# Optimization experiments

Measured on AMD Instinct MI355X. Metric: run time of the kernel, lower is better.

The kernel has to match this reference:

```python
import jax, jax.numpy as jnp
import numpy as np

N, E, IN = 50000, 800000, 128   # nodes, edges, input feature dim
H, C = 8, 32                    # heads, per-head channels
HC = H * C                      # 256 = concat width
NEG_SLOPE = 0.2
BN_EPS = 1e-5


def _gat_conv(x, src, dst, W, a_src, a_dst, b, heads, out_ch, concat):
    """PyG-style GATConv (eval mode, self-loops already in src/dst)."""
    n = x.shape[0]
    h = (x @ W).reshape(n, heads, out_ch)                 # [N,H,C]
    alpha_s = (h * a_src).sum(-1)                         # [N,H]
    alpha_d = (h * a_dst).sum(-1)                         # [N,H]
    e = jax.nn.leaky_relu(alpha_s[src] + alpha_d[dst], NEG_SLOPE)  # [Etot,H]
    # segment softmax over destination nodes (every node has a self-loop)
    emax = jax.ops.segment_max(e, dst, num_segments=n)    # [N,H]
    e = jnp.exp(e - emax[dst])
    denom = jax.ops.segment_sum(e, dst, num_segments=n)
    alpha = e / (denom[dst] + 1e-16)                      # [Etot,H]
    msg = h[src] * alpha[:, :, None]                      # [Etot,H,C]
    out = jax.ops.segment_sum(msg, dst, num_segments=n)   # [N,H,C]
    out = out.reshape(n, heads * out_ch) if concat else out.mean(axis=1)
    return out + b


def _bn(y, g, beta, m, v):
    return (y - m) * jax.lax.rsqrt(v + BN_EPS) * g + beta


def setup_inputs() -> dict:
    key = jax.random.key(0)
    ks = jax.random.split(key, 32)
    def p(i, shape, s=0.1):
        return jax.random.normal(ks[i], shape, dtype=jnp.float32) * s
    x = jax.random.normal(ks[0], (N, IN), dtype=jnp.float32)
    edge_index = jax.random.randint(ks[1], (2, E), 0, N, dtype=jnp.int32)
    d = dict(
        x=x, edge_index=edge_index,
        W1=p(2, (IN, HC)), a_src1=p(3, (H, C)), a_dst1=p(4, (H, C)), b1=p(5, (HC,)),
        bn1_g=jnp.ones((HC,), jnp.float32), bn1_b=jnp.zeros((HC,), jnp.float32),
        bn1_m=p(6, (HC,)), bn1_v=jax.random.uniform(ks[7], (HC,), jnp.float32, 0.5, 1.5),
        W2=p(8, (HC, HC)), a_src2=p(9, (H, C)), a_dst2=p(10, (H, C)), b2=p(11, (HC,)),
        bn2_g=jnp.ones((HC,), jnp.float32), bn2_b=jnp.zeros((HC,), jnp.float32),
        bn2_m=p(12, (HC,)), bn2_v=jax.random.uniform(ks[13], (HC,), jnp.float32, 0.5, 1.5),
        W3=p(14, (HC, C)), a_src3=p(15, (1, C)), a_dst3=p(16, (1, C)), b3=p(17, (C,)),
        Ws1=p(18, (IN, HC)), bs1=p(19, (HC,)),
        Ws2=p(20, (HC, C)), bs2=p(21, (C,)),
    )
    return d


def reference(x, edge_index, W1, a_src1, a_dst1, b1, bn1_g, bn1_b, bn1_m, bn1_v,
              W2, a_src2, a_dst2, b2, bn2_g, bn2_b, bn2_m, bn2_v,
              W3, a_src3, a_dst3, b3, Ws1, bs1, Ws2, bs2):
    n = x.shape[0]
    loops = jnp.arange(n, dtype=edge_index.dtype)
    src = jnp.concatenate([edge_index[0], loops])   # PyG add_self_loops=True
    dst = jnp.concatenate([edge_index[1], loops])
    x0 = x @ Ws1 + bs1                               # skip1
    h = _gat_conv(x, src, dst, W1, a_src1, a_dst1, b1, H, C, True)
    h = jax.nn.elu(_bn(h, bn1_g, bn1_b, bn1_m, bn1_v)) + x0
    xs = h @ Ws2 + bs2                               # skip2
    h2 = _gat_conv(h, src, dst, W2, a_src2, a_dst2, b2, H, C, True)
    h2 = jax.nn.elu(_bn(h2, bn2_g, bn2_b, bn2_m, bn2_v))
    out = _gat_conv(h2, src, dst, W3, a_src3, a_dst3, b3, 1, C, False) + xs
    return out
```

## Files before the change

### kernel.cpp

```cpp
#include <hip/hip_runtime.h>
#include <hip/hip_bf16.h>

#define NEG_SLOPE 0.2f
#define BN_EPS 1e-5f
#define BSH 8
#define STASH_CAP 6400

typedef __attribute__((ext_vector_type(8))) short bf16x8;
typedef __attribute__((ext_vector_type(4))) float f32x4;
typedef __attribute__((ext_vector_type(2))) float f32x2;

#if defined(__has_builtin)
#if __has_builtin(__builtin_amdgcn_cvt_f32_fp8) && __has_builtin(__builtin_amdgcn_cvt_pk_fp8_f32)
#define HW_FP8 1
#endif
#if __has_builtin(__builtin_amdgcn_cvt_pk_f32_fp8)
#define HW_FP8_PK 1
#endif
#endif

__device__ __forceinline__ float bf2f(unsigned short u) {
    union { unsigned int i; float f; } x;
    x.i = ((unsigned int)u) << 16;
    return x.f;
}
__device__ __forceinline__ unsigned short f2bf(float f) {
    __hip_bfloat16 b = __float2bfloat16(f);
    return *reinterpret_cast<unsigned short*>(&b);
}
__device__ __forceinline__ float lrelu(float v) {
    return v > 0.f ? v : NEG_SLOPE * v;
}
__device__ __forceinline__ void gload_lds16(const void* g, void* l) {
    __builtin_amdgcn_global_load_lds(
        (const __attribute__((address_space(1))) unsigned int*)(g),
        (__attribute__((address_space(3))) unsigned int*)(l),
        16, 0, 0);
}

__device__ __forceinline__ unsigned char f8enc(float f) {
#ifdef HW_FP8
    int p = __builtin_amdgcn_cvt_pk_fp8_f32(f, 0.f, 0, false);
    return (unsigned char)(p & 0xff);
#else
    float a = fabsf(f);
    unsigned int sign = (__float_as_uint(f) >> 31) << 7;
    if (a < 0.0009765625f) return (unsigned char)sign;
    a = fminf(a, 448.f);
    unsigned int bits = __float_as_uint(a);
    int e = (int)((bits >> 23) & 0xff) - 127;
    unsigned int mant = bits & 0x7fffff;
    if (e < -6) {
        int q = (int)(a * 512.f + 0.5f);
        if (q >= 8) return (unsigned char)(sign | 0x08);
        return (unsigned char)(sign | q);
    }
    unsigned int m = mant >> 20;
    unsigned int rem = mant & 0xfffff;
    if (rem > 0x80000 || (rem == 0x80000 && (m & 1))) m++;
    if (m == 8) { m = 0; e++; }
    if (e > 8) { e = 8; m = 6; }
    return (unsigned char)(sign | ((unsigned int)(e + 7) << 3) | m);
#endif
}
template <int SEL>
__device__ __forceinline__ float f8dec(unsigned int w) {
#ifdef HW_FP8
    return __builtin_amdgcn_cvt_f32_fp8(w, SEL);
#else
    unsigned int b = (w >> (SEL * 8)) & 0xff;
    unsigned int s = b >> 7, em = b & 0x7f;
    float mag;
    if (em >= 8) {
        unsigned int bits = (((em >> 3) + 120) << 23) | ((em & 7) << 20);
        mag = __uint_as_float(bits);
    } else {
        mag = (float)em * 0.001953125f;
    }
    return s ? -mag : mag;
#endif
}
__device__ __forceinline__ void fma_f8x4(float we, unsigned int wv, float4& acc) {
#ifdef HW_FP8_PK
    f32x2 lo = __builtin_amdgcn_cvt_pk_f32_fp8((int)wv, false);
    f32x2 hi = __builtin_amdgcn_cvt_pk_f32_fp8((int)wv, true);
    acc.x = fmaf(we, lo[0], acc.x);
    acc.y = fmaf(we, lo[1], acc.y);
    acc.z = fmaf(we, hi[0], acc.z);
    acc.w = fmaf(we, hi[1], acc.w);
#else
    acc.x = fmaf(we, f8dec<0>(wv), acc.x);
    acc.y = fmaf(we, f8dec<1>(wv), acc.y);
    acc.z = fmaf(we, f8dec<2>(wv), acc.z);
    acc.w = fmaf(we, f8dec<3>(wv), acc.w);
#endif
}

__device__ __forceinline__ int block_scan_incl(int v, int t) {
    int lane = t & 63, w = t >> 6;
    int sv = v;
    #pragma unroll
    for (int off = 1; off < 64; off <<= 1) {
        int u = __shfl_up(sv, off);
        if (lane >= off) sv += u;
    }
    __shared__ int ws_[4];
    if (lane == 63) ws_[w] = sv;
    __syncthreads();
    if (t == 0) {
        int a = 0;
        #pragma unroll
        for (int k = 0; k < 4; k++) { int x = ws_[k]; ws_[k] = a; a += x; }
    }
    __syncthreads();
    return sv + ws_[w];
}

__global__ __launch_bounds__(256) void phase1(const int* __restrict__ dstl,
                                              int E, int N, int NB,
                                              int* __restrict__ gHist,
                                              const float* __restrict__ x,
                                              unsigned short* __restrict__ xb, int n4x,
                                              const float* __restrict__ W1,
                                              const float* __restrict__ Ws1,
                                              const float* __restrict__ W2,
                                              const float* __restrict__ Ws2,
                                              const float* __restrict__ W3,
                                              const float* __restrict__ a_src1,
                                              const float* __restrict__ a_dst1,
                                              const float* __restrict__ a_src2,
                                              const float* __restrict__ a_dst2,
                                              const float* __restrict__ a_src3,
                                              const float* __restrict__ a_dst3,
                                              unsigned short* __restrict__ Wcat1,
                                              unsigned short* __restrict__ Wcat2,
                                              unsigned short* __restrict__ W3t) {
    int t = threadIdx.x;
    if (blockIdx.x < 256) {
        __shared__ int h[256];
        h[t] = 0;
        __syncthreads();
        int Etot = E + N;
        for (int i = blockIdx.x * 256 + t; i < Etot; i += 256 * 256) {
            int d = (i < E) ? dstl[i] : (i - E);
            atomicAdd(&h[d >> BSH], 1);
        }
        __syncthreads();
        if (t < NB && h[t]) atomicAdd(&gHist[t], h[t]);
        return;
    }
    int i = (blockIdx.x - 256) * 256 + t;
    if (i < n4x) {
        float4 v = reinterpret_cast<const float4*>(x)[i];
        ushort4 o;
        o.x = f2bf(v.x); o.y = f2bf(v.y); o.z = f2bf(v.z); o.w = f2bf(v.w);
        reinterpret_cast<ushort4*>(xb)[i] = o;
        return;
    }
    int j = i - n4x;
    if (j < 32768) {
        int m = j >> 7, k = j & 127;
        Wcat1[j] = f2bf(W1[k * 256 + m]);
    } else if (j < 65536) {
        int q = j - 32768; int m = q >> 7, k = q & 127;
        Wcat1[32768 + q] = f2bf(Ws1[k * 256 + m]);
    } else if (j < 131072) {
        int q = j - 65536; int m = q >> 8, k = q & 255;
        Wcat2[q] = f2bf(W2[k * 256 + m]);
    } else if (j < 139264) {
        int q = j - 131072; int m = q >> 8, k = q & 255;
        Wcat2[65536 + q] = f2bf(Ws2[k * 32 + m]);
    } else if (j < 147456) {
        int q = j - 139264; int m = q >> 8, k = q & 255;
        W3t[q] = f2bf(W3[k * 32 + m]);
    } else if (j < 149504) {
        int q = j - 147456; int r = q >> 7, k = q & 127;
        int h = r & 7;
        const float* av = (r < 8) ? a_src1 : a_dst1;
        float s = 0.f;
        #pragma unroll
        for (int c = 0; c < 32; c++) s += W1[k * 256 + h * 32 + c] * av[h * 32 + c];
        Wcat1[(512 + r) * 128 + k] = f2bf(s);
    } else if (j < 153600) {
        int q = j - 149504; int r = q >> 8, k = q & 255;
        int h = r & 7;
        const float* av = (r < 8) ? a_src2 : a_dst2;
        float s = 0.f;
        #pragma unroll
        for (int c = 0; c < 32; c++) s += W2[k * 256 + h * 32 + c] * av[h * 32 + c];
        Wcat2[(288 + r) * 256 + k] = f2bf(s);
    } else if (j < 154112) {
        int q = j - 153600; int r = q >> 8, k = q & 255;
        const float* av = r ? a_dst3 : a_src3;
        float s = 0.f;
        #pragma unroll
        for (int c = 0; c < 32; c++) s += W3[k * 32 + c] * av[c];
        W3t[(32 + r) * 256 + k] = f2bf(s);
    }
}

__global__ __launch_bounds__(256) void bucket_scatter(const int* __restrict__ srcl,
                                                      const int* __restrict__ dstl,
                                                      int E, int N, int NB,
                                                      const int* __restrict__ gHist,
                                                      int* __restrict__ gCursor,
                                                      unsigned int* __restrict__ bktEdges) {
    __shared__ unsigned int stage[4096];
    __shared__ int lbase[256];
    __shared__ int hist[256];
    __shared__ int bexcl[257];
    __shared__ int curk[256];
    __shared__ int gbase[256];
    int t = threadIdx.x;
    int Etot = E + N;
    int begin = blockIdx.x * 4096;

    int gv = (t < NB) ? gHist[t] : 0;
    int gincl = block_scan_incl(gv, t);
    lbase[t] = gincl - gv;
    __syncthreads();

    hist[t] = 0;
    __syncthreads();

    unsigned int ent[16];
    int eb[16];
    #pragma unroll
    for (int k = 0; k < 16; k++) {
        int i = begin + k * 256 + t;
        if (i < Etot) {
            int s, d;
            if (i < E) { s = srcl[i]; d = dstl[i]; }
            else       { s = d = i - E; }
            eb[k] = d >> BSH;
            ent[k] = ((unsigned int)s << BSH) | (unsigned int)(d & 255);
            atomicAdd(&hist[eb[k]], 1);
        } else eb[k] = -1;
    }
    __syncthreads();

    int v = hist[t];
    int incl = block_scan_incl(v, t);
    bexcl[t] = incl - v;
    curk[t] = incl - v;
    if (t == 255) bexcl[256] = incl;
    __syncthreads();

    #pragma unroll
    for (int k = 0; k < 16; k++) {
        if (eb[k] >= 0) {
            int slot = atomicAdd(&curk[eb[k]], 1);
            stage[slot] = ent[k];
        }
    }
    if (t < NB) {
        int cnt = hist[t];
        gbase[t] = cnt ? (lbase[t] + atomicAdd(&gCursor[t], cnt)) : 0;
    }
    __syncthreads();

    int total = bexcl[256];
    for (int p = t; p < total; p += 256) {
        int lo = 0, hi = NB - 1;
        while (lo < hi) {
            int mid = (lo + hi + 1) >> 1;
            if (bexcl[mid] <= p) lo = mid; else hi = mid - 1;
        }
        bktEdges[gbase[lo] + (p - bexcl[lo])] = stage[p];
    }
}

__global__ __launch_bounds__(256) void bucket_to_csr(const unsigned int* __restrict__ bktEdges,
                                                     const int* __restrict__ gHist,
                                                     int* __restrict__ indptr,
                                                     int* __restrict__ esrc,
                                                     int N, int NB, int Etot) {
    __shared__ int lbase[256];
    __shared__ int nh[256];
    __shared__ int ncur[256];
    __shared__ unsigned int stash[STASH_CAP];
    int b = blockIdx.x, t = threadIdx.x;

    int gv = (t < NB) ? gHist[t] : 0;
    int gincl = block_scan_incl(gv, t);
    lbase[t] = gincl - gv;
    __syncthreads();
    int base = lbase[b];
    int cnt = gHist[b];
    int nodeBase = b << BSH;

    nh[t] = 0;
    __syncthreads();
    for (int p = t; p < cnt; p += 256) {
        unsigned int e = bktEdges[base + p];
        if (p < STASH_CAP) stash[p] = e;
        atomicAdd(&nh[e & 255], 1);
    }
    __syncthreads();
    int v = nh[t];
    int incl = block_scan_incl(v, t);
    int excl = incl - v;
    ncur[t] = excl;
    if (nodeBase + t < N) indptr[nodeBase + t] = base + excl;
    __syncthreads();
    for (int p = t; p < cnt; p += 256) {
        unsigned int e = (p < STASH_CAP) ? stash[p] : bktEdges[base + p];
        int slot = atomicAdd(&ncur[e & 255], 1);
        esrc[base + slot] = (int)(e >> BSH);
    }
    if (b == 0 && t == 0) indptr[N] = Etot;
}

template <int K, int COLS>
__global__ __launch_bounds__(256) void gemm_panel(const unsigned short* __restrict__ A,
                                                  const unsigned short* __restrict__ Bt,
                                                  unsigned short* __restrict__ outBf,
                                                  unsigned char* __restrict__ outQ,
                                                  unsigned short* __restrict__ outSk,
                                                  const float* __restrict__ biasSk,
                                                  float* __restrict__ asOut,
                                                  float* __restrict__ adOut,
                                                  int M, int NCtot,
                                                  int split, int split2,
                                                  int ldBf, int ldSk) {
    constexpr int KS = K / 32;
    constexpr int NJ = COLS / 16;
    constexpr int BYTES = COLS * K * 2;
    constexpr int RB = (K == 128) ? 8 : 9;
    __shared__ __align__(16) char lds[BYTES];

    int t = threadIdx.x;
    int w = t >> 6, lane = t & 63;
    int l16 = lane & 15, quad = lane >> 4;
    int rowBase = blockIdx.x * 64 + w * 16;
    int colBase = blockIdx.y * COLS;

    bf16x8 af[KS];
    {
        int gr = rowBase + l16; if (gr >= M) gr = M - 1;
        const unsigned short* aP = A + (size_t)gr * K + quad * 8;
        #pragma unroll
        for (int ks = 0; ks < KS; ks++)
            af[ks] = *reinterpret_cast<const bf16x8*>(aP + ks * 32);
    }

    {
        const char* bSrc = reinterpret_cast<const char*>(Bt + (size_t)colBase * K);
        #pragma unroll
        for (int i = 0; i < BYTES / 4096; i++) {
            int a = (i * 256 + t) * 16;
            int g = a ^ (((a >> RB) & 15) << 4);
            gload_lds16(bSrc + g, &lds[a]);
        }
    }
    __syncthreads();

    f32x4 acc[NJ];
    #pragma unroll
    for (int j = 0; j < NJ; j++) acc[j] = (f32x4){0.f, 0.f, 0.f, 0.f};

    #pragma unroll
    for (int j = 0; j < NJ; j++) {
        int base = (j * 16 + l16) * (K * 2) + quad * 16;
        #pragma unroll
        for (int ks = 0; ks < KS; ks++) {
            int addr = (base + ks * 64) ^ (l16 << 4);
            bf16x8 b = *reinterpret_cast<const bf16x8*>(&lds[addr]);
            acc[j] = __builtin_amdgcn_mfma_f32_16x16x32_bf16(af[ks], b, acc[j], 0, 0, 0);
        }
    }

    #pragma unroll
    for (int j = 0; j < NJ; j++) {
        int c = colBase + j * 16 + l16;
        if (c >= NCtot) continue;
        if (c < split) {
            #pragma unroll
            for (int r = 0; r < 4; r++) {
                int row = rowBase + quad * 4 + r;
                if (row >= M) continue;
                float v = acc[j][r];
                if (outBf) outBf[(size_t)row * ldBf + c] = f2bf(v);
                if (outQ)  outQ[(size_t)row * ldBf + c] = f8enc(v);
            }
        } else if (c < split2) {
            float bv = biasSk[c - split];
            #pragma unroll
            for (int r = 0; r < 4; r++) {
                int row = rowBase + quad * 4 + r;
                if (row >= M) continue;
                outSk[(size_t)row * ldSk + (c - split)] = f2bf(acc[j][r] + bv);
            }
        } else {
            int a = c - split2;
            #pragma unroll
            for (int r = 0; r < 4; r++) {
                int row = rowBase + quad * 4 + r;
                if (row >= M) continue;
                float v = acc[j][r];
                if (NCtot - split2 == 16) {
                    if (a < 8) asOut[(size_t)row * 8 + a] = v;
                    else       adOut[(size_t)row * 8 + a - 8] = v;
                } else {
                    if (a == 0) asOut[row] = v;
                    else        adOut[row] = v;
                }
            }
        }
    }
}

template <int MODE>
__global__ __launch_bounds__(256) void agg256(const unsigned char* __restrict__ hq,
                                              const float* __restrict__ as,
                                              const float* __restrict__ ad,
                                              const int* __restrict__ indptr,
                                              const int* __restrict__ esrc,
                                              const float* __restrict__ bias,
                                              const float* __restrict__ bn_g,
                                              const float* __restrict__ bn_b,
                                              const float* __restrict__ bn_m,
                                              const float* __restrict__ bn_v,
                                              const unsigned short* __restrict__ skip,
                                              unsigned short* __restrict__ out, int N) {
    int t = threadIdx.x;
    int n = blockIdx.x * 4 + (t >> 6);
    if (n >= N) return;
    int lane = t & 63;
    int e8 = lane >> 3, h8 = lane & 7;
    int g4 = lane >> 4, cl = lane & 15;
    int hd = cl >> 1;
    int start = indptr[n], end = indptr[n + 1];
    int cnt = end - start;

    float adh = ad[n * 8 + h8];
    const unsigned char* hqc = hq + cl * 16;

    float4 acc0 = make_float4(0.f, 0.f, 0.f, 0.f);
    float4 acc1 = make_float4(0.f, 0.f, 0.f, 0.f);
    float4 acc2 = make_float4(0.f, 0.f, 0.f, 0.f);
    float4 acc3 = make_float4(0.f, 0.f, 0.f, 0.f);
    float sm = 0.f;
    int nfull = cnt & ~7;

    int sA = 0, sB = 0;
    float wA = 0.f, wB = 0.f;
    uint4 hv0 = {}, hv1 = {};
    if (nfull) {
        sA = esrc[start + e8];
        wA = __expf(lrelu(as[sA * 8 + h8] + adh));
        int r0 = __shfl(sA, g4 * 8);
        int r1 = __shfl(sA, (4 + g4) * 8);
        hv0 = *reinterpret_cast<const uint4*>(hqc + (size_t)r0 * 256);
        hv1 = *reinterpret_cast<const uint4*>(hqc + (size_t)r1 * 256);
        if (nfull > 8) {
            sB = esrc[start + 8 + e8];
            wB = __expf(lrelu(as[sB * 8 + h8] + adh));
        }
    }
    for (int i0 = start; i0 < start + nfull; i0 += 8) {
        uint4 u0 = hv0, u1 = hv1;
        float wcur = wA;
        if (i0 + 8 < start + nfull) {
            int r0 = __shfl(sB, g4 * 8);
            int r1 = __shfl(sB, (4 + g4) * 8);
            hv0 = *reinterpret_cast<const uint4*>(hqc + (size_t)r0 * 256);
            hv1 = *reinterpret_cast<const uint4*>(hqc + (size_t)r1 * 256);
        }
        sA = sB; wA = wB;
        if (i0 + 16 < start + nfull) {
            sB = esrc[i0 + 16 + e8];
            wB = __expf(lrelu(as[sB * 8 + h8] + adh));
        }
        sm += wcur;
        float w0 = __shfl(wcur, g4 * 8 + hd);
        float w1 = __shfl(wcur, (4 + g4) * 8 + hd);
        fma_f8x4(w0, u0.x, acc0);
        fma_f8x4(w0, u0.y, acc1);
        fma_f8x4(w0, u0.z, acc2);
        fma_f8x4(w0, u0.w, acc3);
        fma_f8x4(w1, u1.x, acc0);
        fma_f8x4(w1, u1.y, acc1);
        fma_f8x4(w1, u1.z, acc2);
        fma_f8x4(w1, u1.w, acc3);
    }
    int rem = cnt - nfull;
    if (rem) {
        int i0 = start + nfull;
        int idx = i0 + e8;
        bool valid = idx < end;
        int s_r = esrc[valid ? idx : end - 1];
        float w_r = valid ? __expf(lrelu(as[s_r * 8 + h8] + adh)) : 0.f;
        sm += w_r;
        int r0 = __shfl(s_r, g4 * 8);
        uint4 u0 = *reinterpret_cast<const uint4*>(hqc + (size_t)r0 * 256);
        float w0 = __shfl(w_r, g4 * 8 + hd);
        fma_f8x4(w0, u0.x, acc0);
        fma_f8x4(w0, u0.y, acc1);
        fma_f8x4(w0, u0.z, acc2);
        fma_f8x4(w0, u0.w, acc3);
        if (rem > 4) {
            int r1 = __shfl(s_r, (4 + g4) * 8);
            uint4 u1 = *reinterpret_cast<const uint4*>(hqc + (size_t)r1 * 256);
            float w1 = __shfl(w_r, (4 + g4) * 8 + hd);
            fma_f8x4(w1, u1.x, acc0);
            fma_f8x4(w1, u1.y, acc1);
            fma_f8x4(w1, u1.z, acc2);
            fma_f8x4(w1, u1.w, acc3);
        }
    }

    acc0.x += __shfl_xor(acc0.x, 16); acc0.y += __shfl_xor(acc0.y, 16);
    acc0.z += __shfl_xor(acc0.z, 16); acc0.w += __shfl_xor(acc0.w, 16);
    acc0.x += __shfl_xor(acc0.x, 32); acc0.y += __shfl_xor(acc0.y, 32);
    acc0.z += __shfl_xor(acc0.z, 32); acc0.w += __shfl_xor(acc0.w, 32);
    acc1.x += __shfl_xor(acc1.x, 16); acc1.y += __shfl_xor(acc1.y, 16);
    acc1.z += __shfl_xor(acc1.z, 16); acc1.w += __shfl_xor(acc1.w, 16);
    acc1.x += __shfl_xor(acc1.x, 32); acc1.y += __shfl_xor(acc1.y, 32);
    acc1.z += __shfl_xor(acc1.z, 32); acc1.w += __shfl_xor(acc1.w, 32);
    acc2.x += __shfl_xor(acc2.x, 16); acc2.y += __shfl_xor(acc2.y, 16);
    acc2.z += __shfl_xor(acc2.z, 16); acc2.w += __shfl_xor(acc2.w, 16);
    acc2.x += __shfl_xor(acc2.x, 32); acc2.y += __shfl_xor(acc2.y, 32);
    acc2.z += __shfl_xor(acc2.z, 32); acc2.w += __shfl_xor(acc2.w, 32);
    acc3.x += __shfl_xor(acc3.x, 16); acc3.y += __shfl_xor(acc3.y, 16);
    acc3.z += __shfl_xor(acc3.z, 16); acc3.w += __shfl_xor(acc3.w, 16);
    acc3.x += __shfl_xor(acc3.x, 32); acc3.y += __shfl_xor(acc3.y, 32);
    acc3.z += __shfl_xor(acc3.z, 32); acc3.w += __shfl_xor(acc3.w, 32);

    #pragma unroll
    for (int off = 8; off < 64; off <<= 1) sm += __shfl_xor(sm, off);
    float il = 1.f / (sm + 1e-16f);
    float il_c = __shfl(il, hd);

    float4 my;
    if (g4 == 0)      my = acc0;
    else if (g4 == 1) my = acc1;
    else if (g4 == 2) my = acc2;
    else              my = acc3;
    int cb = cl * 16 + g4 * 4;

    float4 bv  = *reinterpret_cast<const float4*>(&bias[cb]);
    float4 gv  = *reinterpret_cast<const float4*>(&bn_g[cb]);
    float4 bbv = *reinterpret_cast<const float4*>(&bn_b[cb]);
    float4 mv  = *reinterpret_cast<const float4*>(&bn_m[cb]);
    float4 vv  = *reinterpret_cast<const float4*>(&bn_v[cb]);
    float o[4] = {my.x * il_c + bv.x, my.y * il_c + bv.y,
                  my.z * il_c + bv.z, my.w * il_c + bv.w};
    float g[4] = {gv.x, gv.y, gv.z, gv.w}, bb[4] = {bbv.x, bbv.y, bbv.z, bbv.w};
    float m[4] = {mv.x, mv.y, mv.z, mv.w}, vr[4] = {vv.x, vv.y, vv.z, vv.w};
    float sk[4] = {0.f, 0.f, 0.f, 0.f};
    if (MODE == 1) {
        ushort4 s4 = *reinterpret_cast<const ushort4*>(&skip[(size_t)n * 256 + cb]);
        sk[0] = bf2f(s4.x); sk[1] = bf2f(s4.y); sk[2] = bf2f(s4.z); sk[3] = bf2f(s4.w);
    }
    ushort4 res;
    unsigned short* rp = &res.x;
    #pragma unroll
    for (int j = 0; j < 4; j++) {
        float val = (o[j] - m[j]) * rsqrtf(vr[j] + BN_EPS) * g[j] + bb[j];
        val = val > 0.f ? val : (__expf(val) - 1.f);
        val += sk[j];
        rp[j] = f2bf(val);
    }
    *reinterpret_cast<ushort4*>(&out[(size_t)n * 256 + cb]) = res;
}

__global__ __launch_bounds__(256) void agg32(const unsigned short* __restrict__ h3,
                                             const float* __restrict__ as,
                                             const float* __restrict__ ad,
                                             const int* __restrict__ indptr,
                                             const int* __restrict__ esrc,
                                             const float* __restrict__ b3,
                                             const unsigned short* __restrict__ xs,
                                             float* __restrict__ out, int N) {
    int t = threadIdx.x;
    int n = blockIdx.x * 4 + (t >> 6);
    if (n >= N) return;
    int lane = t & 63;
    int e_sub = lane >> 3, c4 = (lane & 7) * 4;
    int start = indptr[n], end = indptr[n + 1];
    float adn = ad[n];

    float4 acc = make_float4(0.f, 0.f, 0.f, 0.f);
    float sm = 0.f;
    int i0 = start;
    for (; i0 + 16 <= end; i0 += 16) {
        int sA = esrc[i0 + e_sub];
        int sB = esrc[i0 + 8 + e_sub];
        float wA = __expf(lrelu(as[sA] + adn));
        float wB = __expf(lrelu(as[sB] + adn));
        sm += wA + wB;
        ushort4 hA = *reinterpret_cast<const ushort4*>(&h3[(size_t)sA * 32 + c4]);
        ushort4 hB = *reinterpret_cast<const ushort4*>(&h3[(size_t)sB * 32 + c4]);
        acc.x = fmaf(wA, bf2f(hA.x), acc.x); acc.y = fmaf(wA, bf2f(hA.y), acc.y);
        acc.z = fmaf(wA, bf2f(hA.z), acc.z); acc.w = fmaf(wA, bf2f(hA.w), acc.w);
        acc.x = fmaf(wB, bf2f(hB.x), acc.x); acc.y = fmaf(wB, bf2f(hB.y), acc.y);
        acc.z = fmaf(wB, bf2f(hB.z), acc.z); acc.w = fmaf(wB, bf2f(hB.w), acc.w);
    }
    for (; i0 < end; i0 += 8) {
        int idx = i0 + e_sub;
        bool valid = idx < end;
        if (valid) {
            int s = esrc[idx];
            float w = __expf(lrelu(as[s] + adn));
            sm += w;
            ushort4 hv = *reinterpret_cast<const ushort4*>(&h3[(size_t)s * 32 + c4]);
            acc.x = fmaf(w, bf2f(hv.x), acc.x);
            acc.y = fmaf(w, bf2f(hv.y), acc.y);
            acc.z = fmaf(w, bf2f(hv.z), acc.z);
            acc.w = fmaf(w, bf2f(hv.w), acc.w);
        }
    }
    #pragma unroll
    for (int off = 8; off < 64; off <<= 1) {
        sm    += __shfl_xor(sm, off);
        acc.x += __shfl_xor(acc.x, off);
        acc.y += __shfl_xor(acc.y, off);
        acc.z += __shfl_xor(acc.z, off);
        acc.w += __shfl_xor(acc.w, off);
    }
    if (e_sub == 0) {
        float il = 1.f / (sm + 1e-16f);
        float4 bv = *reinterpret_cast<const float4*>(&b3[c4]);
        ushort4 xv = *reinterpret_cast<const ushort4*>(&xs[(size_t)n * 32 + c4]);
        float4 o;
        o.x = acc.x * il + bv.x + bf2f(xv.x);
        o.y = acc.y * il + bv.y + bf2f(xv.y);
        o.z = acc.z * il + bv.z + bf2f(xv.z);
        o.w = acc.w * il + bv.w + bf2f(xv.w);
        *reinterpret_cast<float4*>(&out[(size_t)n * 32 + c4]) = o;
    }
}

extern "C" void kernel_launch(void* const* d_in, const int* in_sizes, int n_in,
                              void* d_out, int out_size, void* d_ws, size_t ws_size,
                              hipStream_t stream) {
    const float* x      = (const float*)d_in[0];
    const int*   eidx   = (const int*)  d_in[1];
    const float* W1     = (const float*)d_in[2];
    const float* a_src1 = (const float*)d_in[3];
    const float* a_dst1 = (const float*)d_in[4];
    const float* b1     = (const float*)d_in[5];
    const float* bn1_g  = (const float*)d_in[6];
    const float* bn1_b  = (const float*)d_in[7];
    const float* bn1_m  = (const float*)d_in[8];
    const float* bn1_v  = (const float*)d_in[9];
    const float* W2     = (const float*)d_in[10];
    const float* a_src2 = (const float*)d_in[11];
    const float* a_dst2 = (const float*)d_in[12];
    const float* b2     = (const float*)d_in[13];
    const float* bn2_g  = (const float*)d_in[14];
    const float* bn2_b  = (const float*)d_in[15];
    const float* bn2_m  = (const float*)d_in[16];
    const float* bn2_v  = (const float*)d_in[17];
    const float* W3     = (const float*)d_in[18];
    const float* a_src3 = (const float*)d_in[19];
    const float* a_dst3 = (const float*)d_in[20];
    const float* b3     = (const float*)d_in[21];
    const float* Ws1    = (const float*)d_in[22];
    const float* bs1    = (const float*)d_in[23];
    const float* Ws2    = (const float*)d_in[24];
    const float* bs2    = (const float*)d_in[25];

    const int N = in_sizes[0] / 128;
    const int E = in_sizes[1] / 2;
    const int Etot = E + N;
    const int NB = (N + 255) >> 8;
    const int* srcl = eidx;
    const int* dstl = eidx + E;

    char* ws = (char*)d_ws;
    size_t off = 0;
    auto alloc = [&](size_t bytes) -> void* {
        void* p = ws + off;
        off += (bytes + 255) & ~(size_t)255;
        return p;
    };
    unsigned short* xb    = (unsigned short*)alloc((size_t)N * 128 * 2);
    unsigned short* feat  = (unsigned short*)alloc((size_t)N * 256 * 2);
    unsigned char*  hq    = (unsigned char*)alloc((size_t)N * 256);
    unsigned short* h2b   = (unsigned short*)alloc((size_t)N * 256 * 2);
    unsigned short* featb = (unsigned short*)alloc((size_t)N * 256 * 2);
    unsigned short* xsbuf = (unsigned short*)alloc((size_t)N * 32 * 2);
    unsigned short* h3b   = (unsigned short*)alloc((size_t)N * 32 * 2);
    float*          asb   = (float*)alloc((size_t)N * 8 * 4);
    float*          adb   = (float*)alloc((size_t)N * 8 * 4);
    unsigned short* Wcat1 = (unsigned short*)alloc((size_t)640 * 128 * 2);
    unsigned short* Wcat2 = (unsigned short*)alloc((size_t)320 * 256 * 2);
    unsigned short* W3t   = (unsigned short*)alloc((size_t)64 * 256 * 2);
    int* gHC     = (int*)alloc(512 * 4);
    int* gHist   = gHC;
    int* gCursor = gHC + 256;
    unsigned int* bktEdges = (unsigned int*)alloc((size_t)Etot * 4);
    int* indptr  = (int*)alloc((size_t)(N + 1) * 4);
    int* esrc    = (int*)alloc((size_t)Etot * 4);
    (void)ws_size; (void)n_in; (void)out_size;

    hipMemsetAsync(gHC, 0, 512 * 4, stream);
    int n4x = N * 128 / 4;
    int prepBlocks = (n4x + 154112 + 255) / 256;
    phase1<<<256 + prepBlocks, 256, 0, stream>>>(dstl, E, N, NB, gHist,
                                                 x, xb, n4x,
                                                 W1, Ws1, W2, Ws2, W3,
                                                 a_src1, a_dst1, a_src2, a_dst2,
                                                 a_src3, a_dst3,
                                                 Wcat1, Wcat2, W3t);
    bucket_scatter<<<(Etot + 4095) / 4096, 256, 0, stream>>>(srcl, dstl, E, N, NB,
                                                             gHist, gCursor, bktEdges);
    bucket_to_csr<<<NB, 256, 0, stream>>>(bktEdges, gHist, indptr, esrc, N, NB, Etot);

    int gy64 = (N + 63) / 64;
    int gn4 = (N + 3) / 4;

    gemm_panel<128, 128><<<dim3(gy64, 5), 256, 0, stream>>>(xb, Wcat1, nullptr, hq, feat, bs1,
                                                            asb, adb,
                                                            N, 528, 256, 512, 256, 256);
    agg256<1><<<gn4, 256, 0, stream>>>(hq, asb, adb, indptr, esrc, b1,
                                       bn1_g, bn1_b, bn1_m, bn1_v, feat, h2b, N);

    gemm_panel<256, 64><<<dim3(gy64, 5), 256, 0, stream>>>(h2b, Wcat2, nullptr, hq, xsbuf, bs2,
                                                           asb, adb,
                                                           N, 304, 256, 288, 256, 32);
    agg256<0><<<gn4, 256, 0, stream>>>(hq, asb, adb, indptr, esrc, b2,
                                       bn2_g, bn2_b, bn2_m, bn2_v, nullptr, featb, N);

    gemm_panel<256, 64><<<dim3(gy64, 1), 256, 0, stream>>>(featb, W3t, h3b, nullptr, nullptr, nullptr,
                                                           asb, adb,
                                                           N, 34, 32, 32, 32, 32);
    agg32<<<gn4, 256, 0, stream>>>(h3b, asb, adb, indptr, esrc, b3, xsbuf,
                                   (float*)d_out, N);
}
```

Before: 351.8 us.

## Replace two-level bucket CSR build with per-node count, scan, and atomic scatter

The CSR construction is restructured. Per-node in-degree counts are now taken with global atomics in phase1, a per-bucket scan writes indptr and a cursor array, and a simple edge_scatter kernel places each source with one global atomic per edge. This drops the staged bucket_scatter and bucket_to_csr passes and the intermediate bktEdges buffer. In exchange it adds about 850k global atomics in both the histogram and the scatter, scatter writes become random, and the order of edges within each node becomes nondeterministic, which can change floating-point summation order.

```diff
diff --git a/kernel.cpp b/kernel.cpp
--- a/kernel.cpp
+++ b/kernel.cpp
@@ -4,7 +4,6 @@
 #define NEG_SLOPE 0.2f
 #define BN_EPS 1e-5f
 #define BSH 8
-#define STASH_CAP 6400
 
 typedef __attribute__((ext_vector_type(8))) short bf16x8;
 typedef __attribute__((ext_vector_type(4))) float f32x4;
@@ -119,6 +118,7 @@
 __global__ __launch_bounds__(256) void phase1(const int* __restrict__ dstl,
                                               int E, int N, int NB,
                                               int* __restrict__ gHist,
+                                              int* __restrict__ nodeCnt,
                                               const float* __restrict__ x,
                                               unsigned short* __restrict__ xb, int n4x,
                                               const float* __restrict__ W1,
@@ -144,6 +144,7 @@
         for (int i = blockIdx.x * 256 + t; i < Etot; i += 256 * 256) {
             int d = (i < E) ? dstl[i] : (i - E);
             atomicAdd(&h[d >> BSH], 1);
+            atomicAdd(&nodeCnt[d], 1);
         }
         __syncthreads();
         if (t < NB && h[t]) atomicAdd(&gHist[t], h[t]);
@@ -199,116 +200,42 @@
     }
 }
 
-__global__ __launch_bounds__(256) void bucket_scatter(const int* __restrict__ srcl,
-                                                      const int* __restrict__ dstl,
-                                                      int E, int N, int NB,
-                                                      const int* __restrict__ gHist,
-                                                      int* __restrict__ gCursor,
-                                                      unsigned int* __restrict__ bktEdges) {
-    __shared__ unsigned int stage[4096];
+__global__ __launch_bounds__(256) void node_scan(const int* __restrict__ gHist,
+                                                 const int* __restrict__ nodeCnt,
+                                                 int* __restrict__ indptr,
+                                                 int* __restrict__ cursor,
+                                                 int N, int NB, int Etot) {
+    int b = blockIdx.x, t = threadIdx.x;
     __shared__ int lbase[256];
-    __shared__ int hist[256];
-    __shared__ int bexcl[257];
-    __shared__ int curk[256];
-    __shared__ int gbase[256];
-    int t = threadIdx.x;
-    int Etot = E + N;
-    int begin = blockIdx.x * 4096;
-
-    int gv = (t < NB) ? gHist[t] : 0;
-    int gincl = block_scan_incl(gv, t);
-    lbase[t] = gincl - gv;
-    __syncthreads();
-
-    hist[t] = 0;
-    __syncthreads();
-
-    unsigned int ent[16];
-    int eb[16];
-    #pragma unroll
-    for (int k = 0; k < 16; k++) {
-        int i = begin + k * 256 + t;
-        if (i < Etot) {
-            int s, d;
-            if (i < E) { s = srcl[i]; d = dstl[i]; }
-            else       { s = d = i - E; }
-            eb[k] = d >> BSH;
-            ent[k] = ((unsigned int)s << BSH) | (unsigned int)(d & 255);
-            atomicAdd(&hist[eb[k]], 1);
-        } else eb[k] = -1;
-    }
-    __syncthreads();
-
-    int v = hist[t];
-    int incl = block_scan_incl(v, t);
-    bexcl[t] = incl - v;
-    curk[t] = incl - v;
-    if (t == 255) bexcl[256] = incl;
-    __syncthreads();
-
-    #pragma unroll
-    for (int k = 0; k < 16; k++) {
-        if (eb[k] >= 0) {
-            int slot = atomicAdd(&curk[eb[k]], 1);
-            stage[slot] = ent[k];
-        }
-    }
-    if (t < NB) {
-        int cnt = hist[t];
-        gbase[t] = cnt ? (lbase[t] + atomicAdd(&gCursor[t], cnt)) : 0;
-    }
-    __syncthreads();
-
-    int total = bexcl[256];
-    for (int p = t; p < total; p += 256) {
-        int lo = 0, hi = NB - 1;
-        while (lo < hi) {
-            int mid = (lo + hi + 1) >> 1;
-            if (bexcl[mid] <= p) lo = mid; else hi = mid - 1;
-        }
-        bktEdges[gbase[lo] + (p - bexcl[lo])] = stage[p];
-    }
-}
-
-__global__ __launch_bounds__(256) void bucket_to_csr(const unsigned int* __restrict__ bktEdges,
-                                                     const int* __restrict__ gHist,
-                                                     int* __restrict__ indptr,
-                                                     int* __restrict__ esrc,
-                                                     int N, int NB, int Etot) {
-    __shared__ int lbase[256];
-    __shared__ int nh[256];
-    __shared__ int ncur[256];
-    __shared__ unsigned int stash[STASH_CAP];
-    int b = blockIdx.x, t = threadIdx.x;
-
     int gv = (t < NB) ? gHist[t] : 0;
     int gincl = block_scan_incl(gv, t);
     lbase[t] = gincl - gv;
     __syncthreads();
     int base = lbase[b];
-    int cnt = gHist[b];
-    int nodeBase = b << BSH;
-
-    nh[t] = 0;
-    __syncthreads();
-    for (int p = t; p < cnt; p += 256) {
-        unsigned int e = bktEdges[base + p];
-        if (p < STASH_CAP) stash[p] = e;
-        atomicAdd(&nh[e & 255], 1);
-    }
-    __syncthreads();
-    int v = nh[t];
+    int node = (b << BSH) + t;
+    int v = (node < N) ? nodeCnt[node] : 0;
     int incl = block_scan_incl(v, t);
     int excl = incl - v;
-    ncur[t] = excl;
-    if (nodeBase + t < N) indptr[nodeBase + t] = base + excl;
-    __syncthreads();
-    for (int p = t; p < cnt; p += 256) {
-        unsigned int e = (p < STASH_CAP) ? stash[p] : bktEdges[base + p];
-        int slot = atomicAdd(&ncur[e & 255], 1);
-        esrc[base + slot] = (int)(e >> BSH);
+    if (node < N) {
+        indptr[node] = base + excl;
+        cursor[node] = base + excl;
     }
     if (b == 0 && t == 0) indptr[N] = Etot;
+}
+
+__global__ __launch_bounds__(256) void edge_scatter(const int* __restrict__ srcl,
+                                                    const int* __restrict__ dstl,
+                                                    int E, int N,
+                                                    int* __restrict__ cursor,
+                                                    int* __restrict__ esrc) {
+    int i = blockIdx.x * 256 + threadIdx.x;
+    int Etot = E + N;
+    if (i >= Etot) return;
+    int s, d;
+    if (i < E) { s = srcl[i]; d = dstl[i]; }
+    else       { s = d = i - E; }
+    int slot = atomicAdd(&cursor[d], 1);
+    esrc[slot] = s;
 }
 
 template <int K, int COLS>
@@ -688,26 +615,25 @@
     unsigned short* Wcat1 = (unsigned short*)alloc((size_t)640 * 128 * 2);
     unsigned short* Wcat2 = (unsigned short*)alloc((size_t)320 * 256 * 2);
     unsigned short* W3t   = (unsigned short*)alloc((size_t)64 * 256 * 2);
-    int* gHC     = (int*)alloc(512 * 4);
-    int* gHist   = gHC;
-    int* gCursor = gHC + 256;
-    unsigned int* bktEdges = (unsigned int*)alloc((size_t)Etot * 4);
+    int* gHN     = (int*)alloc((size_t)(256 + N) * 4);
+    int* gHist   = gHN;
+    int* nodeCnt = gHN + 256;
+    int* cursor  = (int*)alloc((size_t)N * 4);
     int* indptr  = (int*)alloc((size_t)(N + 1) * 4);
     int* esrc    = (int*)alloc((size_t)Etot * 4);
     (void)ws_size; (void)n_in; (void)out_size;
 
-    hipMemsetAsync(gHC, 0, 512 * 4, stream);
+    hipMemsetAsync(gHN, 0, (size_t)(256 + N) * 4, stream);
     int n4x = N * 128 / 4;
     int prepBlocks = (n4x + 154112 + 255) / 256;
-    phase1<<<256 + prepBlocks, 256, 0, stream>>>(dstl, E, N, NB, gHist,
+    phase1<<<256 + prepBlocks, 256, 0, stream>>>(dstl, E, N, NB, gHist, nodeCnt,
                                                  x, xb, n4x,
                                                  W1, Ws1, W2, Ws2, W3,
                                                  a_src1, a_dst1, a_src2, a_dst2,
                                                  a_src3, a_dst3,
                                                  Wcat1, Wcat2, W3t);
-    bucket_scatter<<<(Etot + 4095) / 4096, 256, 0, stream>>>(srcl, dstl, E, N, NB,
-                                                             gHist, gCursor, bktEdges);
-    bucket_to_csr<<<NB, 256, 0, stream>>>(bktEdges, gHist, indptr, esrc, N, NB, Etot);
+    node_scan<<<NB, 256, 0, stream>>>(gHist, nodeCnt, indptr, cursor, N, NB, Etot);
+    edge_scatter<<<(Etot + 255) / 256, 256, 0, stream>>>(srcl, dstl, E, N, cursor, esrc);
 
     int gy64 = (N + 63) / 64;
     int gn4 = (N + 3) / 4;
```

Result: slower. 403.3 us (+14.6%).
